# Kernel tuning notes

Measured on AMD Instinct MI355X. Metric: run time of the kernel, lower is better.

## Reference

```python
import jax, jax.numpy as jnp
import numpy as np

INPUT_DIM = 10              # number of binary covariates in x
N = 2_000_000               # batch size
C = 2 ** (INPUT_DIM + 1)    # 2048 (t, x) combinations, one Linear(1,1) each


def setup_inputs() -> dict:
    key = jax.random.key(0)
    kx, kt, ky, kw, kb = jax.random.split(key, 5)
    x = jax.random.randint(kx, (N, INPUT_DIM), 0, 2).astype(jnp.float32)  # binary covariates
    t = jax.random.randint(kt, (N, 1), 0, 2).astype(jnp.float32)          # binary treatment
    y = jax.random.normal(ky, (N, 1), dtype=jnp.float32)                  # outcome
    # Per-combination Linear(1,1): weight w[i] and bias b[i] for q_z_dummies[i]
    w = jax.random.normal(kw, (C,), dtype=jnp.float32) * 0.5
    b = jax.random.normal(kb, (C,), dtype=jnp.float32) * 0.5
    return {"x": x, "t": t, "y": y, "w": w, "b": b}


def reference(x, t, y, w, b):
    # The torch loop sums (w_i*y + b_i) * [exact match of (t, x) with combination i].
    # Exactly one combination matches per row, so this equals a gather at the
    # combination index. itertools.product([0,1], repeat=d+1) orders bits
    # (t, x_0, ..., x_{d-1}) with the FIRST bit most significant.
    powers = (2 ** jnp.arange(INPUT_DIM - 1, -1, -1)).astype(x.dtype)      # [d]
    idx = (t[:, 0] * (2 ** INPUT_DIM) + x @ powers).astype(jnp.int32)      # [N]
    z_logits = y * w[idx][:, None] + b[idx][:, None]                       # [N, 1]
    # Original returns (z_mu=0, z_var=0, z_logits) in binary mode; z_logits is
    # the only tensor output.
    return z_logits
```

## Files before the change

kernel.cpp:

```cpp
#include <hip/hip_runtime.h>
#include <hip/hip_bf16.h>


#define INPUT_DIM 10
#define ROWS_PER_BLOCK 512

__global__ __launch_bounds__(256) void enc_kernel(
    const float* __restrict__ x,
    const float* __restrict__ t,
    const float* __restrict__ y,
    const float* __restrict__ w,
    const float* __restrict__ b,
    float* __restrict__ out,
    int n)
{
    __shared__ __align__(16) float xs[ROWS_PER_BLOCK * INPUT_DIM];

    const int base = blockIdx.x * ROWS_PER_BLOCK;
    const int rows = (n - base < ROWS_PER_BLOCK) ? (n - base) : ROWS_PER_BLOCK;
    const int dw_valid = rows * INPUT_DIM;
    const float* gx = x + (size_t)base * INPUT_DIM;

#pragma unroll
    for (int k = 0; k < 5; ++k) {
        int d = (threadIdx.x + k * 256) * 4;
        if (d + 4 <= dw_valid) {
            *(float4*)&xs[d] = *(const float4*)&gx[d];
        } else if (d < dw_valid) {
            for (int j = d; j < dw_valid; ++j) xs[j] = gx[j];
        }
    }
    __syncthreads();

    for (int r = threadIdx.x; r < rows; r += 256) {
        const int g = base + r;
        const float* xr = &xs[r * INPUT_DIM];

        float s0 = fmaf(xr[0], 512.f, t[g] * 1024.f);
        float s1 = fmaf(xr[1], 256.f, xr[2] * 128.f);
        float s2 = fmaf(xr[3],  64.f, xr[4] *  32.f);
        float s3 = fmaf(xr[5],  16.f, xr[6] *   8.f);
        float s4 = fmaf(xr[7],   4.f, xr[8] *   2.f);
        float s5 = s4 + xr[9];
        int idx = (int)((s0 + s1) + (s2 + s3) + s5);

        out[g] = fmaf(y[g], w[idx], b[idx]);
    }
}

extern "C" void kernel_launch(void* const* d_in, const int* in_sizes, int n_in,
                              void* d_out, int out_size, void* d_ws, size_t ws_size,
                              hipStream_t stream) {
    const float* x = (const float*)d_in[0];
    const float* t = (const float*)d_in[1];
    const float* y = (const float*)d_in[2];
    const float* w = (const float*)d_in[3];
    const float* b = (const float*)d_in[4];
    float* out = (float*)d_out;

    int n = out_size;
    int grid = (n + ROWS_PER_BLOCK - 1) / ROWS_PER_BLOCK;
    enc_kernel<<<grid, 256, 0, stream>>>(x, t, y, w, b, out, n);
}
```

Before: 136.5 us.

## Stage w/b table in LDS, process two rows per thread with bit-extracted index

Each block now copies the 2048-entry w and b tables into shared memory as interleaved float2 pairs, so the per-row gather hits LDS instead of global/L2. Blocks grow to 512 threads and 1024 rows, and each thread handles two adjacent rows with vectorized float2 loads of t and y and a float2 store. The index is built from exponent bit 29 of each 0/1 float rather than with float multiply-adds. In exchange every block reloads 16KB of table data, and the bit trick is only correct for inputs that are exactly 0.0 or 1.0.

```diff
diff --git a/kernel.cpp b/kernel.cpp
--- a/kernel.cpp
+++ b/kernel.cpp
@@ -1,11 +1,15 @@
 #include <hip/hip_runtime.h>
-#include <hip/hip_bf16.h>
 
 
 #define INPUT_DIM 10
-#define ROWS_PER_BLOCK 512
+#define THREADS 512
+#define ROWS_PER_BLOCK 1024
 
-__global__ __launch_bounds__(256) void enc_kernel(
+__device__ __forceinline__ int fbit(float f) {
+    return (int)((__float_as_uint(f) >> 29) & 1u);
+}
+
+__global__ __launch_bounds__(THREADS) void enc_kernel(
     const float* __restrict__ x,
     const float* __restrict__ t,
     const float* __restrict__ y,
@@ -14,37 +18,76 @@
     float* __restrict__ out,
     int n)
 {
-    __shared__ __align__(16) float xs[ROWS_PER_BLOCK * INPUT_DIM];
+    __shared__ __align__(16) float  xs[ROWS_PER_BLOCK * INPUT_DIM];
+    __shared__ __align__(16) float2 wb[2048];
 
+    const int tid  = threadIdx.x;
     const int base = blockIdx.x * ROWS_PER_BLOCK;
     const int rows = (n - base < ROWS_PER_BLOCK) ? (n - base) : ROWS_PER_BLOCK;
     const int dw_valid = rows * INPUT_DIM;
     const float* gx = x + (size_t)base * INPUT_DIM;
 
+    {
+        const int j = tid * 4;
+        float4 w4 = *(const float4*)&w[j];
+        float4 b4 = *(const float4*)&b[j];
+        wb[j + 0] = make_float2(w4.x, b4.x);
+        wb[j + 1] = make_float2(w4.y, b4.y);
+        wb[j + 2] = make_float2(w4.z, b4.z);
+        wb[j + 3] = make_float2(w4.w, b4.w);
+    }
+
 #pragma unroll
     for (int k = 0; k < 5; ++k) {
-        int d = (threadIdx.x + k * 256) * 4;
+        int d = (tid + k * THREADS) * 4;
         if (d + 4 <= dw_valid) {
             *(float4*)&xs[d] = *(const float4*)&gx[d];
         } else if (d < dw_valid) {
             for (int j = d; j < dw_valid; ++j) xs[j] = gx[j];
         }
     }
+
+    const int r0 = 2 * tid;
+    const int g0 = base + r0;
+    const bool pair   = (r0 + 1 < rows);
+    const bool single = (r0 < rows) && !pair;
+    float2 tv = make_float2(0.f, 0.f), yv = make_float2(0.f, 0.f);
+    if (pair) {
+        tv = *(const float2*)&t[g0];
+        yv = *(const float2*)&y[g0];
+    } else if (single) {
+        tv.x = t[g0];
+        yv.x = y[g0];
+    }
+
     __syncthreads();
 
-    for (int r = threadIdx.x; r < rows; r += 256) {
-        const int g = base + r;
-        const float* xr = &xs[r * INPUT_DIM];
+    if (r0 >= rows) return;
 
-        float s0 = fmaf(xr[0], 512.f, t[g] * 1024.f);
-        float s1 = fmaf(xr[1], 256.f, xr[2] * 128.f);
-        float s2 = fmaf(xr[3],  64.f, xr[4] *  32.f);
-        float s3 = fmaf(xr[5],  16.f, xr[6] *   8.f);
-        float s4 = fmaf(xr[7],   4.f, xr[8] *   2.f);
-        float s5 = s4 + xr[9];
-        int idx = (int)((s0 + s1) + (s2 + s3) + s5);
+    const float4* xp = (const float4*)&xs[r0 * INPUT_DIM];
+    float4 q0 = xp[0], q1 = xp[1], q2 = xp[2], q3 = xp[3], q4 = xp[4];
 
-        out[g] = fmaf(y[g], w[idx], b[idx]);
+    int idx0 = (fbit(tv.x) << 10)
+             | (fbit(q0.x) << 9) | (fbit(q0.y) << 8)
+             | (fbit(q0.z) << 7) | (fbit(q0.w) << 6)
+             | (fbit(q1.x) << 5) | (fbit(q1.y) << 4)
+             | (fbit(q1.z) << 3) | (fbit(q1.w) << 2)
+             | (fbit(q2.x) << 1) |  fbit(q2.y);
+
+    if (pair) {
+        int idx1 = (fbit(tv.y) << 10)
+                 | (fbit(q2.z) << 9) | (fbit(q2.w) << 8)
+                 | (fbit(q3.x) << 7) | (fbit(q3.y) << 6)
+                 | (fbit(q3.z) << 5) | (fbit(q3.w) << 4)
+                 | (fbit(q4.x) << 3) | (fbit(q4.y) << 2)
+                 | (fbit(q4.z) << 1) |  fbit(q4.w);
+        float2 c0 = wb[idx0];
+        float2 c1 = wb[idx1];
+        *(float2*)&out[g0] = make_float2(fmaf(yv.x, c0.x, c0.y),
+                                         fmaf(yv.y, c1.x, c1.y));
+    } else {
+        float2 c0 = wb[idx0];
+        out[g0] = fmaf(yv.x, c0.x, c0.y);
     }
 }
 
@@ -60,5 +103,5 @@
 
     int n = out_size;
     int grid = (n + ROWS_PER_BLOCK - 1) / ROWS_PER_BLOCK;
-    enc_kernel<<<grid, 256, 0, stream>>>(x, t, y, w, b, out, n);
+    enc_kernel<<<grid, THREADS, 0, stream>>>(x, t, y, w, b, out, n);
 }
```

New measurement: 136.1 us. No clear change (-0.3%).

## Build wave-level index bitmasks with ballots and stage weight/bias pairs in LDS

Applied to the files above, without the earlier changes.

Each wave now loads 128 rows of x as coalesced 32-bit words and turns each value into one bit with a ballot. The ballot masks go to shared memory, and each lane extracts the 10-bit window for its two rows and bit-reverses it to form the combination index. The treatment bit is read straight from the float exponent bits. Weights and biases are interleaved into one LDS float2 table per block, so each row does a single LDS lookup instead of two global gathers. This removes the per-row float arithmetic and staging of x through shared memory. In exchange, every block reloads the 16 KB table, and the float-bit tests assume inputs are exactly 0.0 or 1.0.

```diff
diff --git a/kernel.cpp b/kernel.cpp
--- a/kernel.cpp
+++ b/kernel.cpp
@@ -1,11 +1,15 @@
 #include <hip/hip_runtime.h>
-#include <hip/hip_bf16.h>
 
 
 #define INPUT_DIM 10
+#define THREADS 256
+#define WAVES_PB 4
+#define ROWS_PER_WAVE 128
 #define ROWS_PER_BLOCK 512
 
-__global__ __launch_bounds__(256) void enc_kernel(
+__device__ __forceinline__ uint32_t fbitu(uint32_t u) { return (u >> 29) & 1u; }
+
+__global__ __launch_bounds__(THREADS) void enc_kernel(
     const float* __restrict__ x,
     const float* __restrict__ t,
     const float* __restrict__ y,
@@ -14,37 +18,82 @@
     float* __restrict__ out,
     int n)
 {
-    __shared__ __align__(16) float xs[ROWS_PER_BLOCK * INPUT_DIM];
+    __shared__ __align__(16) float2 wb[2048];
+    __shared__ unsigned long long bal[WAVES_PB][21];
 
-    const int base = blockIdx.x * ROWS_PER_BLOCK;
-    const int rows = (n - base < ROWS_PER_BLOCK) ? (n - base) : ROWS_PER_BLOCK;
-    const int dw_valid = rows * INPUT_DIM;
-    const float* gx = x + (size_t)base * INPUT_DIM;
+    const int tid = threadIdx.x;
 
-#pragma unroll
-    for (int k = 0; k < 5; ++k) {
-        int d = (threadIdx.x + k * 256) * 4;
-        if (d + 4 <= dw_valid) {
-            *(float4*)&xs[d] = *(const float4*)&gx[d];
-        } else if (d < dw_valid) {
-            for (int j = d; j < dw_valid; ++j) xs[j] = gx[j];
-        }
+    {
+        const int j = tid * 8;
+        const float4 w0 = *(const float4*)&w[j];
+        const float4 w1 = *(const float4*)&w[j + 4];
+        const float4 b0 = *(const float4*)&b[j];
+        const float4 b1 = *(const float4*)&b[j + 4];
+        wb[j + 0] = make_float2(w0.x, b0.x);
+        wb[j + 1] = make_float2(w0.y, b0.y);
+        wb[j + 2] = make_float2(w0.z, b0.z);
+        wb[j + 3] = make_float2(w0.w, b0.w);
+        wb[j + 4] = make_float2(w1.x, b1.x);
+        wb[j + 5] = make_float2(w1.y, b1.y);
+        wb[j + 6] = make_float2(w1.z, b1.z);
+        wb[j + 7] = make_float2(w1.w, b1.w);
     }
     __syncthreads();
 
-    for (int r = threadIdx.x; r < rows; r += 256) {
-        const int g = base + r;
-        const float* xr = &xs[r * INPUT_DIM];
+    const int wave = tid >> 6;
+    const int lane = tid & 63;
+    const long long rowbase =
+        (long long)blockIdx.x * ROWS_PER_BLOCK + (long long)wave * ROWS_PER_WAVE;
+    if (rowbase >= n) return;
 
-        float s0 = fmaf(xr[0], 512.f, t[g] * 1024.f);
-        float s1 = fmaf(xr[1], 256.f, xr[2] * 128.f);
-        float s2 = fmaf(xr[3],  64.f, xr[4] *  32.f);
-        float s3 = fmaf(xr[5],  16.f, xr[6] *   8.f);
-        float s4 = fmaf(xr[7],   4.f, xr[8] *   2.f);
-        float s5 = s4 + xr[9];
-        int idx = (int)((s0 + s1) + (s2 + s3) + s5);
+    if (rowbase + ROWS_PER_WAVE <= (long long)n) {
+        const uint32_t* xu = (const uint32_t*)x + rowbase * INPUT_DIM;
 
-        out[g] = fmaf(y[g], w[idx], b[idx]);
+        uint32_t v[20];
+#pragma unroll
+        for (int k = 0; k < 20; ++k) v[k] = xu[k * 64 + lane];
+
+        const int g = (int)rowbase + 2 * lane;
+        const float2 tv = *(const float2*)&t[g];
+        const float2 yv = *(const float2*)&y[g];
+
+        unsigned long long s[20];
+#pragma unroll
+        for (int k = 0; k < 20; ++k) s[k] = __ballot(v[k] != 0u);
+
+        if (lane == 0) {
+#pragma unroll
+            for (int k = 0; k < 20; ++k) bal[wave][k] = s[k];
+            bal[wave][20] = 0ull;
+        }
+        asm volatile("s_waitcnt lgkmcnt(0)" ::: "memory");
+
+        const int bo = 20 * lane;
+        const int j0 = bo >> 6;
+        const int sh = bo & 63;
+        unsigned long long lo = bal[wave][j0];
+        unsigned long long hi = bal[wave][j0 + 1];
+        unsigned long long wnd = lo >> sh;
+        if (sh) wnd |= hi << (64 - sh);
+
+        const uint32_t f0 = (uint32_t)wnd & 0x3FFu;
+        const uint32_t f1 = (uint32_t)(wnd >> 10) & 0x3FFu;
+        const int idx0 = (int)((__brev(f0) >> 22) | (fbitu(__float_as_uint(tv.x)) << 10));
+        const int idx1 = (int)((__brev(f1) >> 22) | (fbitu(__float_as_uint(tv.y)) << 10));
+
+        const float2 c0 = wb[idx0];
+        const float2 c1 = wb[idx1];
+        *(float2*)&out[g] = make_float2(fmaf(yv.x, c0.x, c0.y),
+                                        fmaf(yv.y, c1.x, c1.y));
+    } else {
+        for (long long r = rowbase + lane; r < (long long)n; r += 64) {
+            const uint32_t* xr = (const uint32_t*)x + r * INPUT_DIM;
+            uint32_t id = fbitu(__float_as_uint(t[r])) << 10;
+#pragma unroll
+            for (int j = 0; j < INPUT_DIM; ++j) id |= fbitu(xr[j]) << (9 - j);
+            const float2 c = wb[id];
+            out[r] = fmaf(y[r], c.x, c.y);
+        }
     }
 }
 
@@ -60,5 +109,5 @@
 
     int n = out_size;
     int grid = (n + ROWS_PER_BLOCK - 1) / ROWS_PER_BLOCK;
-    enc_kernel<<<grid, 256, 0, stream>>>(x, t, y, w, b, out, n);
+    enc_kernel<<<grid, THREADS, 0, stream>>>(x, t, y, w, b, out, n);
 }
```

Measured after the change: 134.2 us. No clear change (-1.7%).
